# Kernel tuning notes

Hardware: AMD Instinct MI355X
Metric: run time of the kernel (lower is better)

## Reference

```python
import jax, jax.numpy as jnp
import numpy as np

N_A, N_B, D, E = 100000, 100000, 128, 600000
LN_EPS = 1e-5


def _segment_mean(x, seg, num_segments):
    # scatter_mean: sum per segment / count, 0 for empty segments
    sums = jax.ops.segment_sum(x, seg, num_segments=num_segments)
    cnt = jax.ops.segment_sum(jnp.ones((x.shape[0],), x.dtype), seg, num_segments=num_segments)
    return sums / jnp.maximum(cnt, 1.0)[:, None]


def _layer_norm(x, g, b):
    mu = jnp.mean(x, axis=-1, keepdims=True)
    var = jnp.var(x, axis=-1, keepdims=True)
    return (x - mu) * jax.lax.rsqrt(var + LN_EPS) * g + b


def setup_inputs() -> dict:
    key = jax.random.key(0)
    ks = jax.random.split(key, 16)
    scale = 1.0 / np.sqrt(2 * D)  # nn.Linear default uniform bound
    inp = {
        "h_a": jax.random.normal(ks[0], (N_A, D), jnp.float32),
        "h_b": jax.random.normal(ks[1], (N_B, D), jnp.float32),
        "ei_ab": jax.random.randint(ks[2], (2, E), 0, 100000, jnp.int64 if jax.config.jax_enable_x64 else jnp.int32),
        "ei_ba": jax.random.randint(ks[3], (2, E), 0, 100000, jnp.int64 if jax.config.jax_enable_x64 else jnp.int32),
        "ei_aa": jax.random.randint(ks[4], (2, E), 0, 100000, jnp.int64 if jax.config.jax_enable_x64 else jnp.int32),
        "W_ab": jax.random.uniform(ks[5], (D, 2 * D), jnp.float32, -scale, scale),
        "b_ab": jax.random.uniform(ks[6], (D,), jnp.float32, -scale, scale),
        "W_ba": jax.random.uniform(ks[7], (D, 2 * D), jnp.float32, -scale, scale),
        "b_ba": jax.random.uniform(ks[8], (D,), jnp.float32, -scale, scale),
        "W_aa": jax.random.uniform(ks[9], (D, 2 * D), jnp.float32, -scale, scale),
        "b_aa": jax.random.uniform(ks[10], (D,), jnp.float32, -scale, scale),
        "g_a": jnp.ones((D,), jnp.float32),
        "be_a": jnp.zeros((D,), jnp.float32),
        "g_b": jnp.ones((D,), jnp.float32),
        "be_b": jnp.zeros((D,), jnp.float32),
    }
    return inp


def reference(h_a, h_b, ei_ab, ei_ba, ei_aa, W_ab, b_ab, W_ba, b_ba, W_aa, b_aa, g_a, be_a, g_b, be_b):
    # per-edge-type: gather source feats, scatter_mean to dest, linear([dst, agg]), accumulate
    def et_msg(xs, xd, ei, W, b):
        s, d = ei[0], ei[1]
        agg = _segment_mean(xs[s], d, xd.shape[0])  # [N_dst, D]
        return jnp.concatenate([xd, agg], axis=-1) @ W.T + b

    out_a = jnp.zeros_like(h_a)
    out_b = jnp.zeros_like(h_b)
    out_b = out_b + et_msg(h_a, h_b, ei_ab, W_ab, b_ab)   # ('a','to','b')
    out_a = out_a + et_msg(h_b, h_a, ei_ba, W_ba, b_ba)   # ('b','to','a')
    out_a = out_a + et_msg(h_a, h_a, ei_aa, W_aa, b_aa)   # ('a','self','a')

    # norm (dropout is identity in eval / for the deterministic reference)
    out_a = _layer_norm(out_a, g_a, be_a)
    out_b = _layer_norm(out_b, g_b, be_b)
    return out_a, out_b
```

## Files before the change

### kernel.cpp

```cpp
#include <hip/hip_runtime.h>
#include <hip/hip_bf16.h>

#define DD 128
#define KTOT 256
#define CAP 32

typedef __attribute__((ext_vector_type(8))) short short8;
typedef __attribute__((ext_vector_type(4))) float f32x4;

__device__ __forceinline__ unsigned short f2b(float f) {
    union { float f; unsigned u; } x; x.f = f;
    unsigned r = x.u + 0x7FFFu + ((x.u >> 16) & 1u);
    return (unsigned short)(r >> 16);
}

__global__ void bucket_kernel(const int* __restrict__ ei, int E,
                              int* __restrict__ deg, int* __restrict__ bucket)
{
    const int e = blockIdx.x * blockDim.x + threadIdx.x;
    if (e < E) {
        const int s = ei[e];
        const int d = ei[E + e];
        const int pos = atomicAdd(deg + d, 1);
        if (pos < CAP) bucket[(long)d * CAP + pos] = s;
    }
}

__global__ __launch_bounds__(256) void gather_kernel(
    const float* __restrict__ xs, const int* __restrict__ deg,
    const int* __restrict__ bucket, unsigned short* __restrict__ S, int N)
{
    const int lane = threadIdx.x & 63;
    const int wid  = (blockIdx.x * blockDim.x + threadIdx.x) >> 6;
    const int nw   = (gridDim.x * blockDim.x) >> 6;
    for (int d = wid; d < N; d += nw) {
        const int dg = deg[d];
        const int m  = dg < CAP ? dg : CAP;
        const int* bk = bucket + (long)d * CAP;
        float2 a0 = {0.f, 0.f}, a1 = {0.f, 0.f};
        int j = 0;
        for (; j + 2 <= m; j += 2) {
            const int s0 = bk[j], s1 = bk[j + 1];
            const float2 v0 = *(const float2*)(xs + (long)s0 * DD + lane * 2);
            const float2 v1 = *(const float2*)(xs + (long)s1 * DD + lane * 2);
            a0.x += v0.x; a0.y += v0.y;
            a1.x += v1.x; a1.y += v1.y;
        }
        if (j < m) {
            const int s0 = bk[j];
            const float2 v0 = *(const float2*)(xs + (long)s0 * DD + lane * 2);
            a0.x += v0.x; a0.y += v0.y;
        }
        const float inv = 1.0f / (float)(dg > 1 ? dg : 1);
        const float mx = (a0.x + a1.x) * inv;
        const float my = (a0.y + a1.y) * inv;
        const unsigned pk = (unsigned)f2b(mx) | ((unsigned)f2b(my) << 16);
        *(unsigned*)(S + (long)d * DD + lane * 2) = pk;
    }
}

template<bool ACC, bool LN>
__global__ __launch_bounds__(256) void gemm_ln_kernel(
    const float* __restrict__ xd, const unsigned short* __restrict__ S,
    const float* __restrict__ W, const float* __restrict__ bias,
    const float* __restrict__ g, const float* __restrict__ be,
    float* __restrict__ out, int N)
{
    __shared__ unsigned char wlds[64 * 1024];
    const int tid = threadIdx.x;

    {
        const int j = tid >> 1;
        const int k0 = (tid & 1) * 128;
        const float* wr = W + j * KTOT + k0;
        for (int c = 0; c < 16; ++c) {
            const int k = c * 8;
            const float4 u = *(const float4*)(wr + k);
            const float4 v = *(const float4*)(wr + k + 4);
            uint4 p;
            p.x = (unsigned)f2b(u.x) | ((unsigned)f2b(u.y) << 16);
            p.y = (unsigned)f2b(u.z) | ((unsigned)f2b(u.w) << 16);
            p.z = (unsigned)f2b(v.x) | ((unsigned)f2b(v.y) << 16);
            p.w = (unsigned)f2b(v.z) | ((unsigned)f2b(v.w) << 16);
            const int byteoff = j * 512 + ((2 * (k0 + k)) ^ ((j & 7) << 4));
            *(uint4*)(wlds + byteoff) = p;
        }
    }
    __syncthreads();

    const int wave = tid >> 6;
    const int lane = tid & 63;
    const int r16  = lane & 15;
    const int kb   = (lane >> 4) * 8;
    const long rbase = (long)blockIdx.x * 64 + wave * 16;
    const long arow  = rbase + r16;
    const bool rowok = arow < N;

    const float*          xrow = xd + arow * DD;
    const unsigned short* srow = S  + arow * DD;

    f32x4 acc[8];
    #pragma unroll
    for (int i = 0; i < 8; ++i) acc[i] = (f32x4){0.f, 0.f, 0.f, 0.f};

    #pragma unroll
    for (int ks = 0; ks < 8; ++ks) {
        const int kg = ks * 32 + kb;
        short8 af = (short8){0,0,0,0,0,0,0,0};
        if (rowok) {
            if (kg < DD) {
                const float4 u = *(const float4*)(xrow + kg);
                const float4 v = *(const float4*)(xrow + kg + 4);
                af[0] = (short)f2b(u.x); af[1] = (short)f2b(u.y);
                af[2] = (short)f2b(u.z); af[3] = (short)f2b(u.w);
                af[4] = (short)f2b(v.x); af[5] = (short)f2b(v.y);
                af[6] = (short)f2b(v.z); af[7] = (short)f2b(v.w);
            } else {
                af = *(const short8*)(srow + (kg - DD));
            }
        }
        #pragma unroll
        for (int ct = 0; ct < 8; ++ct) {
            const int c = ct * 16 + r16;
            const int byteoff = c * 512 + ((2 * kg) ^ ((c & 7) << 4));
            const short8 bf = *(const short8*)(wlds + byteoff);
            acc[ct] = __builtin_amdgcn_mfma_f32_16x16x32_bf16(af, bf, acc[ct], 0, 0, 0);
        }
    }

    const int qbase = (lane >> 4) * 4;
    #pragma unroll
    for (int ct = 0; ct < 8; ++ct) {
        const int c = ct * 16 + r16;
        const float bb = bias[c];
        #pragma unroll
        for (int q = 0; q < 4; ++q) {
            const long r = rbase + qbase + q;
            float vv = acc[ct][q] + bb;
            if (ACC) { if (r < N) vv += out[r * DD + c]; }
            acc[ct][q] = vv;
        }
    }

    if (LN) {
        #pragma unroll
        for (int q = 0; q < 4; ++q) {
            float s1 = 0.f;
            #pragma unroll
            for (int ct = 0; ct < 8; ++ct) s1 += acc[ct][q];
            s1 += __shfl_xor(s1, 1); s1 += __shfl_xor(s1, 2);
            s1 += __shfl_xor(s1, 4); s1 += __shfl_xor(s1, 8);
            const float mu = s1 * (1.0f / 128.0f);
            float s2 = 0.f;
            #pragma unroll
            for (int ct = 0; ct < 8; ++ct) { const float d = acc[ct][q] - mu; s2 += d * d; }
            s2 += __shfl_xor(s2, 1); s2 += __shfl_xor(s2, 2);
            s2 += __shfl_xor(s2, 4); s2 += __shfl_xor(s2, 8);
            const float rstd = rsqrtf(s2 * (1.0f / 128.0f) + 1e-5f);
            #pragma unroll
            for (int ct = 0; ct < 8; ++ct) {
                const int c = ct * 16 + r16;
                acc[ct][q] = (acc[ct][q] - mu) * rstd * g[c] + be[c];
            }
        }
    }

    #pragma unroll
    for (int ct = 0; ct < 8; ++ct) {
        const int c = ct * 16 + r16;
        #pragma unroll
        for (int q = 0; q < 4; ++q) {
            const long r = rbase + qbase + q;
            if (r < N) out[r * DD + c] = acc[ct][q];
        }
    }
}

extern "C" void kernel_launch(void* const* d_in, const int* in_sizes, int n_in,
                              void* d_out, int out_size, void* d_ws, size_t ws_size,
                              hipStream_t stream) {
    const float* h_a  = (const float*)d_in[0];
    const float* h_b  = (const float*)d_in[1];
    const int*   ei_ab = (const int*)d_in[2];
    const int*   ei_ba = (const int*)d_in[3];
    const int*   ei_aa = (const int*)d_in[4];
    const float* W_ab = (const float*)d_in[5];
    const float* b_ab = (const float*)d_in[6];
    const float* W_ba = (const float*)d_in[7];
    const float* b_ba = (const float*)d_in[8];
    const float* W_aa = (const float*)d_in[9];
    const float* b_aa = (const float*)d_in[10];
    const float* g_a  = (const float*)d_in[11];
    const float* be_a = (const float*)d_in[12];
    const float* g_b  = (const float*)d_in[13];
    const float* be_b = (const float*)d_in[14];

    const int NA   = in_sizes[0] / DD;
    const int NB   = in_sizes[1] / DD;
    const int E_ab = in_sizes[2] / 2;
    const int E_ba = in_sizes[3] / 2;
    const int E_aa = in_sizes[4] / 2;

    float* out_a = (float*)d_out;
    float* out_b = (float*)d_out + (long)NA * DD;

    const int NMAX = NA > NB ? NA : NB;
    unsigned short* S = (unsigned short*)d_ws;
    int* deg    = (int*)(S + (long)NMAX * DD);
    int* bucket = deg + NMAX;

    const int TB = 256;
    auto ggrid = [](int n) { return dim3((unsigned)((n + 255) / 256)); };
    auto gemm_grid = [](int N) { return dim3((unsigned)((N + 63) / 64)); };
    const dim3 GATHER_GRID(2048);

    hipMemsetAsync(deg, 0, (size_t)NB * sizeof(int), stream);
    bucket_kernel<<<ggrid(E_ab), TB, 0, stream>>>(ei_ab, E_ab, deg, bucket);
    gather_kernel<<<GATHER_GRID, TB, 0, stream>>>(h_a, deg, bucket, S, NB);
    gemm_ln_kernel<false, true><<<gemm_grid(NB), TB, 0, stream>>>(
        h_b, S, W_ab, b_ab, g_b, be_b, out_b, NB);

    hipMemsetAsync(deg, 0, (size_t)NA * sizeof(int), stream);
    bucket_kernel<<<ggrid(E_ba), TB, 0, stream>>>(ei_ba, E_ba, deg, bucket);
    gather_kernel<<<GATHER_GRID, TB, 0, stream>>>(h_b, deg, bucket, S, NA);
    gemm_ln_kernel<false, false><<<gemm_grid(NA), TB, 0, stream>>>(
        h_a, S, W_ba, b_ba, g_a, be_a, out_a, NA);

    hipMemsetAsync(deg, 0, (size_t)NA * sizeof(int), stream);
    bucket_kernel<<<ggrid(E_aa), TB, 0, stream>>>(ei_aa, E_aa, deg, bucket);
    gather_kernel<<<GATHER_GRID, TB, 0, stream>>>(h_a, deg, bucket, S, NA);
    gemm_ln_kernel<true, true><<<gemm_grid(NA), TB, 0, stream>>>(
        h_a, S, W_aa, b_aa, g_a, be_a, out_a, NA);
}
```

Measured before the change: 646.3 us.

## Merge the two a-destination GEMMs into one K=384 GEMM with pre-summed weights

Folds the 'b to a' and 'a self a' messages into a single GEMM. The shared h_a part of the weights is pre-added and the two aggregates are concatenated along K, which removes one full GEMM pass and the read-modify-write of out_a. A prep kernel converts the weights to bf16 once per call. The GEMM now stages an A panel in LDS, reads weights from global, and uses a single-pass sum/sum-of-squares LayerNorm reduced across waves in LDS. The gather also switches to 16 lanes per row with 16-byte loads, and the second aggregate is staged temporarily in the out_b buffer. The trade-offs are the single-pass variance, which is less numerically robust, and a dependency on out_b being written only after S_aa is consumed.

Result: faster. 541.9 us (-16.2%).

```diff
diff --git a/kernel.cpp b/kernel.cpp
--- a/kernel.cpp
+++ b/kernel.cpp
@@ -2,7 +2,6 @@
 #include <hip/hip_bf16.h>
 
 #define DD 128
-#define KTOT 256
 #define CAP 32
 
 typedef __attribute__((ext_vector_type(8))) short short8;
@@ -12,6 +11,33 @@
     union { float f; unsigned u; } x; x.f = f;
     unsigned r = x.u + 0x7FFFu + ((x.u >> 16) & 1u);
     return (unsigned short)(r >> 16);
+}
+__device__ __forceinline__ unsigned packbf(float a, float b) {
+    return (unsigned)f2b(a) | ((unsigned)f2b(b) << 16);
+}
+
+__global__ __launch_bounds__(256) void prep_kernel(
+    const float* __restrict__ W_ba, const float* __restrict__ W_aa,
+    const float* __restrict__ W_ab, const float* __restrict__ b_ba,
+    const float* __restrict__ b_aa, unsigned* __restrict__ Wcomb,
+    unsigned* __restrict__ Wab, float* __restrict__ bcomb)
+{
+    const int idx = blockIdx.x * 256 + threadIdx.x;
+    if (idx < 128 * 192) {
+        const int r = idx / 192, p = idx - r * 192, k = p * 2;
+        float v0, v1;
+        if (k < 128)      { v0 = W_ba[r*256+k] + W_aa[r*256+k]; v1 = W_ba[r*256+k+1] + W_aa[r*256+k+1]; }
+        else if (k < 256) { v0 = W_ba[r*256+k];                 v1 = W_ba[r*256+k+1]; }
+        else              { v0 = W_aa[r*256+k-128];             v1 = W_aa[r*256+k-127]; }
+        Wcomb[idx] = packbf(v0, v1);
+    } else if (idx < 128 * 192 + 128 * 128) {
+        const int i = idx - 128 * 192;
+        const int r = i >> 7, p = i & 127, k = p * 2;
+        Wab[i] = packbf(W_ab[r*256+k], W_ab[r*256+k+1]);
+    } else if (idx < 128 * 192 + 128 * 128 + 128) {
+        const int j = idx - (128 * 192 + 128 * 128);
+        bcomb[j] = b_ba[j] + b_aa[j];
+    }
 }
 
 __global__ void bucket_kernel(const int* __restrict__ ei, int E,
@@ -30,148 +56,153 @@
     const float* __restrict__ xs, const int* __restrict__ deg,
     const int* __restrict__ bucket, unsigned short* __restrict__ S, int N)
 {
-    const int lane = threadIdx.x & 63;
-    const int wid  = (blockIdx.x * blockDim.x + threadIdx.x) >> 6;
-    const int nw   = (gridDim.x * blockDim.x) >> 6;
-    for (int d = wid; d < N; d += nw) {
+    const int l16 = threadIdx.x & 15;
+    const int g   = (blockIdx.x * 256 + threadIdx.x) >> 4;
+    const int ng  = (gridDim.x * 256) >> 4;
+    for (int d = g; d < N; d += ng) {
         const int dg = deg[d];
         const int m  = dg < CAP ? dg : CAP;
         const int* bk = bucket + (long)d * CAP;
-        float2 a0 = {0.f, 0.f}, a1 = {0.f, 0.f};
+        float4 u0 = {0,0,0,0}, v0 = {0,0,0,0}, u1 = {0,0,0,0}, v1 = {0,0,0,0};
         int j = 0;
         for (; j + 2 <= m; j += 2) {
-            const int s0 = bk[j], s1 = bk[j + 1];
-            const float2 v0 = *(const float2*)(xs + (long)s0 * DD + lane * 2);
-            const float2 v1 = *(const float2*)(xs + (long)s1 * DD + lane * 2);
-            a0.x += v0.x; a0.y += v0.y;
-            a1.x += v1.x; a1.y += v1.y;
+            const float* p0 = xs + (long)bk[j]     * DD + l16 * 8;
+            const float* p1 = xs + (long)bk[j + 1] * DD + l16 * 8;
+            const float4 a = *(const float4*)p0, b = *(const float4*)(p0 + 4);
+            const float4 c = *(const float4*)p1, e = *(const float4*)(p1 + 4);
+            u0.x += a.x; u0.y += a.y; u0.z += a.z; u0.w += a.w;
+            v0.x += b.x; v0.y += b.y; v0.z += b.z; v0.w += b.w;
+            u1.x += c.x; u1.y += c.y; u1.z += c.z; u1.w += c.w;
+            v1.x += e.x; v1.y += e.y; v1.z += e.z; v1.w += e.w;
         }
         if (j < m) {
-            const int s0 = bk[j];
-            const float2 v0 = *(const float2*)(xs + (long)s0 * DD + lane * 2);
-            a0.x += v0.x; a0.y += v0.y;
+            const float* p0 = xs + (long)bk[j] * DD + l16 * 8;
+            const float4 a = *(const float4*)p0, b = *(const float4*)(p0 + 4);
+            u0.x += a.x; u0.y += a.y; u0.z += a.z; u0.w += a.w;
+            v0.x += b.x; v0.y += b.y; v0.z += b.z; v0.w += b.w;
         }
         const float inv = 1.0f / (float)(dg > 1 ? dg : 1);
-        const float mx = (a0.x + a1.x) * inv;
-        const float my = (a0.y + a1.y) * inv;
-        const unsigned pk = (unsigned)f2b(mx) | ((unsigned)f2b(my) << 16);
-        *(unsigned*)(S + (long)d * DD + lane * 2) = pk;
-    }
-}
-
-template<bool ACC, bool LN>
-__global__ __launch_bounds__(256) void gemm_ln_kernel(
-    const float* __restrict__ xd, const unsigned short* __restrict__ S,
-    const float* __restrict__ W, const float* __restrict__ bias,
-    const float* __restrict__ g, const float* __restrict__ be,
-    float* __restrict__ out, int N)
-{
-    __shared__ unsigned char wlds[64 * 1024];
-    const int tid = threadIdx.x;
-
-    {
-        const int j = tid >> 1;
-        const int k0 = (tid & 1) * 128;
-        const float* wr = W + j * KTOT + k0;
-        for (int c = 0; c < 16; ++c) {
-            const int k = c * 8;
-            const float4 u = *(const float4*)(wr + k);
-            const float4 v = *(const float4*)(wr + k + 4);
-            uint4 p;
-            p.x = (unsigned)f2b(u.x) | ((unsigned)f2b(u.y) << 16);
-            p.y = (unsigned)f2b(u.z) | ((unsigned)f2b(u.w) << 16);
-            p.z = (unsigned)f2b(v.x) | ((unsigned)f2b(v.y) << 16);
-            p.w = (unsigned)f2b(v.z) | ((unsigned)f2b(v.w) << 16);
-            const int byteoff = j * 512 + ((2 * (k0 + k)) ^ ((j & 7) << 4));
-            *(uint4*)(wlds + byteoff) = p;
-        }
+        uint4 pk;
+        pk.x = packbf((u0.x + u1.x) * inv, (u0.y + u1.y) * inv);
+        pk.y = packbf((u0.z + u1.z) * inv, (u0.w + u1.w) * inv);
+        pk.z = packbf((v0.x + v1.x) * inv, (v0.y + v1.y) * inv);
+        pk.w = packbf((v0.z + v1.z) * inv, (v0.w + v1.w) * inv);
+        *(uint4*)(S + (long)d * DD + l16 * 8) = pk;
+    }
+}
+
+template<int KS>
+__global__ __launch_bounds__(256, 3) void gemm_ln_kernel(
+    const float* __restrict__ xd, const unsigned short* __restrict__ S1,
+    const unsigned short* __restrict__ S2, const unsigned short* __restrict__ Wb,
+    const float* __restrict__ bias, const float* __restrict__ g,
+    const float* __restrict__ be, float* __restrict__ out, int N)
+{
+    constexpr int K   = KS * 32;
+    constexpr int RB  = K * 2;
+    constexpr int NCH = RB / 16;
+    __shared__ unsigned char panel[64 * RB];
+
+    const int tid  = threadIdx.x;
+    const long rbase = (long)blockIdx.x * 64;
+
+    #pragma unroll
+    for (int it = 0; it < 64 * NCH / 256; ++it) {
+        const int ci   = it * 256 + tid;
+        const int row  = ci / NCH;
+        const int cpos = ci - row * NCH;
+        const long grow = rbase + row;
+        uint4 pk = {0, 0, 0, 0};
+        if (grow < N) {
+            if (cpos < 16) {
+                const int k = cpos * 8;
+                const float4 u = *(const float4*)(xd + grow * DD + k);
+                const float4 v = *(const float4*)(xd + grow * DD + k + 4);
+                pk.x = packbf(u.x, u.y); pk.y = packbf(u.z, u.w);
+                pk.z = packbf(v.x, v.y); pk.w = packbf(v.z, v.w);
+            } else if (cpos < 32) {
+                pk = *(const uint4*)(S1 + grow * DD + (cpos - 16) * 8);
+            } else if (KS == 12) {
+                pk = *(const uint4*)(S2 + grow * DD + (cpos - 32) * 8);
+            }
+        }
+        const int byteoff = row * RB + ((cpos * 16) ^ ((row & 7) << 4));
+        *(uint4*)(panel + byteoff) = pk;
     }
     __syncthreads();
 
-    const int wave = tid >> 6;
-    const int lane = tid & 63;
-    const int r16  = lane & 15;
-    const int kb   = (lane >> 4) * 8;
-    const long rbase = (long)blockIdx.x * 64 + wave * 16;
-    const long arow  = rbase + r16;
-    const bool rowok = arow < N;
-
-    const float*          xrow = xd + arow * DD;
-    const unsigned short* srow = S  + arow * DD;
-
-    f32x4 acc[8];
-    #pragma unroll
-    for (int i = 0; i < 8; ++i) acc[i] = (f32x4){0.f, 0.f, 0.f, 0.f};
-
-    #pragma unroll
-    for (int ks = 0; ks < 8; ++ks) {
-        const int kg = ks * 32 + kb;
-        short8 af = (short8){0,0,0,0,0,0,0,0};
-        if (rowok) {
-            if (kg < DD) {
-                const float4 u = *(const float4*)(xrow + kg);
-                const float4 v = *(const float4*)(xrow + kg + 4);
-                af[0] = (short)f2b(u.x); af[1] = (short)f2b(u.y);
-                af[2] = (short)f2b(u.z); af[3] = (short)f2b(u.w);
-                af[4] = (short)f2b(v.x); af[5] = (short)f2b(v.y);
-                af[6] = (short)f2b(v.z); af[7] = (short)f2b(v.w);
-            } else {
-                af = *(const short8*)(srow + (kg - DD));
-            }
-        }
-        #pragma unroll
-        for (int ct = 0; ct < 8; ++ct) {
-            const int c = ct * 16 + r16;
-            const int byteoff = c * 512 + ((2 * kg) ^ ((c & 7) << 4));
-            const short8 bf = *(const short8*)(wlds + byteoff);
-            acc[ct] = __builtin_amdgcn_mfma_f32_16x16x32_bf16(af, bf, acc[ct], 0, 0, 0);
-        }
-    }
-
-    const int qbase = (lane >> 4) * 4;
-    #pragma unroll
-    for (int ct = 0; ct < 8; ++ct) {
-        const int c = ct * 16 + r16;
-        const float bb = bias[c];
+    const int wave  = tid >> 6;
+    const int lane  = tid & 63;
+    const int r16   = lane & 15;
+    const int khw   = lane >> 4;
+    const int c0    = wave * 32 + r16;
+    const int c1    = c0 + 16;
+
+    f32x4 acc[4][2];
+    #pragma unroll
+    for (int m = 0; m < 4; ++m) { acc[m][0] = (f32x4){0,0,0,0}; acc[m][1] = (f32x4){0,0,0,0}; }
+
+    constexpr int KH = KS / 2;
+    #pragma unroll 1
+    for (int h = 0; h < 2; ++h) {
+        short8 wf[2][KH];
+        #pragma unroll
+        for (int ks2 = 0; ks2 < KH; ++ks2) {
+            const int kg = (h * KH + ks2) * 32 + khw * 8;
+            wf[0][ks2] = *(const short8*)(Wb + c0 * K + kg);
+            wf[1][ks2] = *(const short8*)(Wb + c1 * K + kg);
+        }
+        #pragma unroll
+        for (int ks2 = 0; ks2 < KH; ++ks2) {
+            const int cpos = (h * KH + ks2) * 4 + khw;
+            #pragma unroll
+            for (int m = 0; m < 4; ++m) {
+                const int row = m * 16 + r16;
+                const short8 af = *(const short8*)(panel + row * RB + ((cpos * 16) ^ ((row & 7) << 4)));
+                acc[m][0] = __builtin_amdgcn_mfma_f32_16x16x32_bf16(af, wf[0][ks2], acc[m][0], 0, 0, 0);
+                acc[m][1] = __builtin_amdgcn_mfma_f32_16x16x32_bf16(af, wf[1][ks2], acc[m][1], 0, 0, 0);
+            }
+        }
+    }
+
+    __syncthreads();
+    float* red = (float*)panel;
+    const int qbase = khw * 4;
+    const float bb0 = bias[c0], bb1 = bias[c1];
+    #pragma unroll
+    for (int m = 0; m < 4; ++m) {
         #pragma unroll
         for (int q = 0; q < 4; ++q) {
-            const long r = rbase + qbase + q;
-            float vv = acc[ct][q] + bb;
-            if (ACC) { if (r < N) vv += out[r * DD + c]; }
-            acc[ct][q] = vv;
-        }
-    }
-
-    if (LN) {
+            acc[m][0][q] += bb0;
+            acc[m][1][q] += bb1;
+            float p  = acc[m][0][q] + acc[m][1][q];
+            float sq = acc[m][0][q] * acc[m][0][q] + acc[m][1][q] * acc[m][1][q];
+            p  += __shfl_xor(p, 1);  p  += __shfl_xor(p, 2);  p  += __shfl_xor(p, 4);  p  += __shfl_xor(p, 8);
+            sq += __shfl_xor(sq, 1); sq += __shfl_xor(sq, 2); sq += __shfl_xor(sq, 4); sq += __shfl_xor(sq, 8);
+            if (r16 == 0) {
+                const int row = m * 16 + qbase + q;
+                red[row * 4 + wave]       = p;
+                red[256 + row * 4 + wave] = sq;
+            }
+        }
+    }
+    __syncthreads();
+    const float gg0 = g[c0], gg1 = g[c1], bee0 = be[c0], bee1 = be[c1];
+    #pragma unroll
+    for (int m = 0; m < 4; ++m) {
         #pragma unroll
         for (int q = 0; q < 4; ++q) {
-            float s1 = 0.f;
-            #pragma unroll
-            for (int ct = 0; ct < 8; ++ct) s1 += acc[ct][q];
-            s1 += __shfl_xor(s1, 1); s1 += __shfl_xor(s1, 2);
-            s1 += __shfl_xor(s1, 4); s1 += __shfl_xor(s1, 8);
-            const float mu = s1 * (1.0f / 128.0f);
-            float s2 = 0.f;
-            #pragma unroll
-            for (int ct = 0; ct < 8; ++ct) { const float d = acc[ct][q] - mu; s2 += d * d; }
-            s2 += __shfl_xor(s2, 1); s2 += __shfl_xor(s2, 2);
-            s2 += __shfl_xor(s2, 4); s2 += __shfl_xor(s2, 8);
-            const float rstd = rsqrtf(s2 * (1.0f / 128.0f) + 1e-5f);
-            #pragma unroll
-            for (int ct = 0; ct < 8; ++ct) {
-                const int c = ct * 16 + r16;
-                acc[ct][q] = (acc[ct][q] - mu) * rstd * g[c] + be[c];
-            }
-        }
-    }
-
-    #pragma unroll
-    for (int ct = 0; ct < 8; ++ct) {
-        const int c = ct * 16 + r16;
-        #pragma unroll
-        for (int q = 0; q < 4; ++q) {
-            const long r = rbase + qbase + q;
-            if (r < N) out[r * DD + c] = acc[ct][q];
+            const int row = m * 16 + qbase + q;
+            const float sum = red[row*4+0] + red[row*4+1] + red[row*4+2] + red[row*4+3];
+            const float ssq = red[256+row*4+0] + red[256+row*4+1] + red[256+row*4+2] + red[256+row*4+3];
+            const float mu  = sum * (1.0f / 128.0f);
+            const float var = ssq * (1.0f / 128.0f) - mu * mu;
+            const float rstd = rsqrtf(var + 1e-5f);
+            const long grow = rbase + row;
+            if (grow < N) {
+                out[grow * DD + c0] = (acc[m][0][q] - mu) * rstd * gg0 + bee0;
+                out[grow * DD + c1] = (acc[m][1][q] - mu) * rstd * gg1 + bee1;
+            }
         }
     }
 }
@@ -205,30 +236,34 @@
     float* out_b = (float*)d_out + (long)NA * DD;
 
     const int NMAX = NA > NB ? NA : NB;
-    unsigned short* S = (unsigned short*)d_ws;
-    int* deg    = (int*)(S + (long)NMAX * DD);
+    unsigned short* S_ws = (unsigned short*)d_ws;
+    int* deg    = (int*)(S_ws + (long)NMAX * DD);
     int* bucket = deg + NMAX;
+    unsigned* Wcomb = (unsigned*)(bucket + (long)NMAX * CAP);
+    unsigned* Wab_b = Wcomb + 128 * 192;
+    float* bcomb    = (float*)(Wab_b + 128 * 128);
+    unsigned short* S_aa = (unsigned short*)out_b;
 
     const int TB = 256;
-    auto ggrid = [](int n) { return dim3((unsigned)((n + 255) / 256)); };
-    auto gemm_grid = [](int N) { return dim3((unsigned)((N + 63) / 64)); };
+    auto egrid = [](int n) { return dim3((unsigned)((n + 255) / 256)); };
+    auto ggrid = [](int N) { return dim3((unsigned)((N + 63) / 64)); };
     const dim3 GATHER_GRID(2048);
 
+    prep_kernel<<<161, TB, 0, stream>>>(W_ba, W_aa, W_ab, b_ba, b_aa, Wcomb, Wab_b, bcomb);
+
+    hipMemsetAsync(deg, 0, (size_t)NA * sizeof(int), stream);
+    bucket_kernel<<<egrid(E_ba), TB, 0, stream>>>(ei_ba, E_ba, deg, bucket);
+    gather_kernel<<<GATHER_GRID, TB, 0, stream>>>(h_b, deg, bucket, S_ws, NA);
+    hipMemsetAsync(deg, 0, (size_t)NA * sizeof(int), stream);
+    bucket_kernel<<<egrid(E_aa), TB, 0, stream>>>(ei_aa, E_aa, deg, bucket);
+    gather_kernel<<<GATHER_GRID, TB, 0, stream>>>(h_a, deg, bucket, S_aa, NA);
+    gemm_ln_kernel<12><<<ggrid(NA), TB, 0, stream>>>(
+        h_a, S_ws, S_aa, (const unsigned short*)Wcomb, bcomb, g_a, be_a, out_a, NA);
+
     hipMemsetAsync(deg, 0, (size_t)NB * sizeof(int), stream);
-    bucket_kernel<<<ggrid(E_ab), TB, 0, stream>>>(ei_ab, E_ab, deg, bucket);
-    gather_kernel<<<GATHER_GRID, TB, 0, stream>>>(h_a, deg, bucket, S, NB);
-    gemm_ln_kernel<false, true><<<gemm_grid(NB), TB, 0, stream>>>(
-        h_b, S, W_ab, b_ab, g_b, be_b, out_b, NB);
-
-    hipMemsetAsync(deg, 0, (size_t)NA * sizeof(int), stream);
-    bucket_kernel<<<ggrid(E_ba), TB, 0, stream>>>(ei_ba, E_ba, deg, bucket);
-    gather_kernel<<<GATHER_GRID, TB, 0, stream>>>(h_b, deg, bucket, S, NA);
-    gemm_ln_kernel<false, false><<<gemm_grid(NA), TB, 0, stream>>>(
-        h_a, S, W_ba, b_ba, g_a, be_a, out_a, NA);
-
-    hipMemsetAsync(deg, 0, (size_t)NA * sizeof(int), stream);
-    bucket_kernel<<<ggrid(E_aa), TB, 0, stream>>>(ei_aa, E_aa, deg, bucket);
-    gather_kernel<<<GATHER_GRID, TB, 0, stream>>>(h_a, deg, bucket, S, NA);
-    gemm_ln_kernel<true, true><<<gemm_grid(NA), TB, 0, stream>>>(
-        h_a, S, W_aa, b_aa, g_a, be_a, out_a, NA);
-}
+    bucket_kernel<<<egrid(E_ab), TB, 0, stream>>>(ei_ab, E_ab, deg, bucket);
+    gather_kernel<<<GATHER_GRID, TB, 0, stream>>>(h_a, deg, bucket, S_ws, NB);
+    gemm_ln_kernel<8><<<ggrid(NB), TB, 0, stream>>>(
+        h_b, S_ws, (const unsigned short*)nullptr, (const unsigned short*)Wab_b,
+        b_ab, g_b, be_b, out_b, NB);
+}
```
